# Optimization experiments

Measured on AMD Instinct MI355X. Metric: run time of the kernel, lower is better.

The kernel has to match this reference:

```python
import jax, jax.numpy as jnp
import numpy as np
from jax import lax

B = 8192
HS = 64        # hidden_size (output channels)
HS4 = HS + 4   # internal channel count (68)
K = 3          # conv kernel size


def setup_inputs() -> dict:
    key = jax.random.key(0)
    ks = jax.random.split(key, 16)
    def n(k, shape, s=1.0):
        return jax.random.normal(k, shape, dtype=jnp.float32) * s
    return {
        "x": n(ks[0], (B, HS, 6, 6)),
        "cell": n(ks[1], (B, 2)),
        "interspace_coord": n(ks[2], (B, 2, 6, 6)),
        "conv1_w": n(ks[3], (HS4, HS4, K, K), 0.05),
        "conv1_b": n(ks[4], (HS4,), 0.05),
        "conv3_w": n(ks[5], (HS4, HS4, K, K), 0.05),
        "conv3_b": n(ks[6], (HS4,), 0.05),
        "lin5_w": n(ks[7], (9 * HS, HS4 * 25), 0.02),
        "lin5_b": n(ks[8], (9 * HS,), 0.02),
        "lin4_w": n(ks[9], (9 * HS, HS4 * 16), 0.02),
        "lin4_b": n(ks[10], (9 * HS,), 0.02),
        "lin3_w": n(ks[11], (9 * HS, HS4 * 9), 0.02),
        "lin3_b": n(ks[12], (9 * HS,), 0.02),
        "final_w": n(ks[13], (HS, 9 * HS), 0.02),
        "final_b": n(ks[14], (HS,), 0.02),
    }


def _conv(z, w, b):
    # torch Conv2d with padding=k//2, stride 1 == SAME conv, NCHW/OIHW
    y = lax.conv_general_dilated(z, w, (1, 1), 'SAME',
                                 dimension_numbers=('NCHW', 'OIHW', 'NCHW'))
    return y + b[None, :, None, None]


def _corners(z, ws):
    # four corner windows, stacked on a new leading axis (corner-major)
    H, W = z.shape[-2:]
    return jnp.stack([z[..., :ws, :ws],
                      z[..., :ws, W - ws:],
                      z[..., H - ws:, :ws],
                      z[..., H - ws:, W - ws:]], axis=0)


def reference(x, cell, interspace_coord,
              conv1_w, conv1_b, conv3_w, conv3_b,
              lin5_w, lin5_b, lin4_w, lin4_b, lin3_w, lin3_b,
              final_w, final_b):
    Bn = x.shape[0]
    new_cell = jnp.broadcast_to(cell.reshape(Bn, -1)[:, :, None, None],
                                (Bn, 2, 6, 6))
    lins = {5: (lin5_w, lin5_b), 4: (lin4_w, lin4_b), 3: (lin3_w, lin3_b)}
    for ws in (5, 4, 3):
        z = jnp.concatenate([x, new_cell, interspace_coord], axis=1)  # [B,68,6,6]
        z = _corners(z, ws).reshape(-1, HS4, ws, ws)                  # [4B,68,ws,ws]
        z = jnp.sin(z) + jnp.cos(z)
        z = jax.nn.relu(_conv(z, conv1_w, conv1_b))
        z = jnp.sin(z) + jnp.cos(z)
        z = jax.nn.relu(_conv(z, conv3_w, conv3_b)).reshape(4, Bn, -1)
        Wl, bl = lins[ws]
        z = jax.nn.relu(z @ Wl.T + bl).reshape(4, Bn, HS, 3, 3)
        m = jnp.concatenate([z[0], z[1]], axis=-1)   # [B,64,3,6]
        n = jnp.concatenate([z[2], z[3]], axis=-1)
        x = jnp.concatenate([m, n], axis=-2)          # [B,64,6,6]
    ew = 3
    c = _corners(x, ew)                               # [4,B,64,3,3]
    c = c.reshape(4 * Bn, -1) @ final_w.T + final_b   # [4B,64]
    c = c.reshape(Bn, HS, 2, 2)                       # same flat-order reshape as torch
    xc = x[:, :, ew - 1:ew + 1, ew - 1:ew + 1]        # center 2x2
    return (xc * c).reshape(Bn, HS, -1)
```

## Files before the change

kernel.cpp:

```cpp
#include <hip/hip_runtime.h>
#include <hip/hip_bf16.h>
#include <cstdint>
#include <cstddef>

#define BN 8192
#define MTOT 32768

using bf16 = __hip_bfloat16;
typedef float f32x4 __attribute__((ext_vector_type(4)));
typedef short short8 __attribute__((ext_vector_type(8)));

__device__ __forceinline__ bf16 f2b(float v) { return __float2bfloat16(v); }
__device__ __forceinline__ float b2f(bf16 v) { return __bfloat162float(v); }
__device__ __forceinline__ float sincos_sum(float x) {
    return 1.41421356237f * __sinf(x + 0.78539816340f);
}

template<int WS> struct WsCfg;
template<> struct WsCfg<5> { static constexpr int KD = 1728, NP = 1792, KTRUE = 1700; };
template<> struct WsCfg<4> { static constexpr int KD = 1088, NP = 1152, KTRUE = 1088; };
template<> struct WsCfg<3> { static constexpr int KD = 640,  NP = 640,  KTRUE = 612;  };

__global__ __launch_bounds__(256)
void zprep_block(const float* __restrict__ xF, const float* __restrict__ cell,
                 const float* __restrict__ isc, bf16* __restrict__ Z,
                 int m0g, int CM)
{
    constexpr int KD = 1728, KTRUE = 1700;
    const int b = blockIdx.x, tid = threadIdx.x;
    __shared__ float s[68][37];

    for (int i = tid; i < 64 * 36; i += 256) {
        int ic = i / 36, off = i % 36;
        s[ic][off] = sincos_sum(xF[((size_t)b * 64 + ic) * 36 + off]);
    }
    if (tid < 2) {
        float t = sincos_sum(cell[b * 2 + tid]);
        #pragma unroll
        for (int off = 0; off < 36; off++) s[64 + tid][off] = t;
    }
    if (tid >= 64 && tid < 136) {
        int j = tid - 64;
        int ic = j / 36, off = j % 36;
        s[66 + ic][off] = sincos_sum(isc[((size_t)b * 2 + ic) * 36 + off]);
    }
    __syncthreads();

    for (int i = tid; i < 4 * KD; i += 256) {
        int q = i / KD, k = i % KD;
        int gm = q * BN + b;
        if (gm < m0g || gm >= m0g + CM) continue;
        float v = 0.f;
        if (k < KTRUE) {
            int pi = k / 68, ic = k % 68;
            int r = (q >> 1) + pi / 5;
            int c = (q & 1) + pi % 5;
            v = s[ic][r * 6 + c];
        }
        Z[(size_t)(gm - m0g) * KD + k] = f2b(v);
    }
}

template<int WSv>
__device__ __forceinline__ bf16 conv_elem(const float* __restrict__ src, int n, int k)
{
    constexpr int KTRUE = 68 * WSv * WSv;
    float v = 0.f;
    if (n < KTRUE && k < KTRUE) {
        int po = n / 68, oc = n % 68, ro = po / WSv, co = po % WSv;
        int pi = k / 68, ic = k % 68, ri = pi / WSv, ci = pi % WSv;
        int kr = ri - ro + 1, kc = ci - co + 1;
        if (kr >= 0 && kr < 3 && kc >= 0 && kc < 3)
            v = src[((oc * 68 + ic) * 3 + kr) * 3 + kc];
    }
    return f2b(v);
}
template<int WSv>
__device__ __forceinline__ bf16 lin_elem(const float* __restrict__ wl, int n, int k)
{
    constexpr int KTRUE = 68 * WSv * WSv;
    float v = 0.f;
    if (n < 576 && k < KTRUE) {
        int pi = k / 68, ic = k % 68;
        v = wl[(size_t)n * KTRUE + ic * (WSv * WSv) + pi];
    }
    return f2b(v);
}

__global__ void megabuild(const float* __restrict__ c1w, const float* __restrict__ c3w,
                          const float* __restrict__ l5w, const float* __restrict__ l4w,
                          const float* __restrict__ l3w, const float* __restrict__ fw,
                          const float* __restrict__ c1b, const float* __restrict__ c3b,
                          const float* __restrict__ bl5, const float* __restrict__ bl4,
                          const float* __restrict__ bl3, const float* __restrict__ bfin,
                          const float* __restrict__ cell, const float* __restrict__ isc,
                          bf16* __restrict__ w1d5, bf16* __restrict__ w3d5,
                          bf16* __restrict__ w1d4, bf16* __restrict__ w3d4,
                          bf16* __restrict__ w1d3, bf16* __restrict__ w3d3,
                          bf16* __restrict__ wl5p, bf16* __restrict__ wl4p,
                          bf16* __restrict__ wl3p, bf16* __restrict__ wfp,
                          float* __restrict__ bias,
                          bf16* __restrict__ Z4, bf16* __restrict__ Z3)
{
    constexpr unsigned S0 = 2u*1792*1728, S1 = 2u*1152*1088, S2 = 2u*640*640;
    constexpr unsigned S3 = 640u*1728, S4 = 640u*1088, S5 = 640u*640;
    constexpr unsigned S6 = 128u*576, S7 = 9216;
    constexpr unsigned S8 = 4u*8192*16*4, S9 = 4u*8192*9*4, S10 = 32768u*28;
    constexpr unsigned O1=S0, O2=O1+S1, O3=O2+S2, O4=O3+S3, O5=O4+S4, O6=O5+S5,
                       O7=O6+S6, O8=O7+S7, O9=O8+S8, O10=O9+S9, OT=O10+S10;
    unsigned e = blockIdx.x * 256u + threadIdx.x;
    if (e >= OT) return;
    if (e < O1) {
        constexpr unsigned per = 1792u*1728;
        unsigned i = (e < per) ? e : e - per;
        bf16* dst = (e < per) ? w1d5 : w3d5;
        const float* src = (e < per) ? c1w : c3w;
        dst[i] = conv_elem<5>(src, (int)(i / 1728u), (int)(i % 1728u));
    } else if (e < O2) {
        unsigned i0 = e - O1; constexpr unsigned per = 1152u*1088;
        unsigned i = (i0 < per) ? i0 : i0 - per;
        bf16* dst = (i0 < per) ? w1d4 : w3d4;
        const float* src = (i0 < per) ? c1w : c3w;
        dst[i] = conv_elem<4>(src, (int)(i / 1088u), (int)(i % 1088u));
    } else if (e < O3) {
        unsigned i0 = e - O2; constexpr unsigned per = 640u*640;
        unsigned i = (i0 < per) ? i0 : i0 - per;
        bf16* dst = (i0 < per) ? w1d3 : w3d3;
        const float* src = (i0 < per) ? c1w : c3w;
        dst[i] = conv_elem<3>(src, (int)(i / 640u), (int)(i % 640u));
    } else if (e < O4) {
        unsigned i = e - O3;
        wl5p[i] = lin_elem<5>(l5w, (int)(i / 1728u), (int)(i % 1728u));
    } else if (e < O5) {
        unsigned i = e - O4;
        wl4p[i] = lin_elem<4>(l4w, (int)(i / 1088u), (int)(i % 1088u));
    } else if (e < O6) {
        unsigned i = e - O5;
        wl3p[i] = lin_elem<3>(l3w, (int)(i / 640u), (int)(i % 640u));
    } else if (e < O7) {
        unsigned i = e - O6, n = i / 576u, k = i % 576u;
        wfp[i] = (n < 64u) ? f2b(fw[n * 576u + k]) : f2b(0.f);
    } else if (e < O8) {
        int i = (int)(e - O7);
        float v = 0.f;
        if (i < 1792)      { int n = i;        if (n < 1700) v = c1b[n % 68]; }
        else if (i < 3584) { int n = i - 1792; if (n < 1700) v = c3b[n % 68]; }
        else if (i < 4736) { int n = i - 3584; if (n < 1088) v = c1b[n % 68]; }
        else if (i < 5888) { int n = i - 4736; if (n < 1088) v = c3b[n % 68]; }
        else if (i < 6528) { int n = i - 5888; if (n < 612)  v = c1b[n % 68]; }
        else if (i < 7168) { int n = i - 6528; if (n < 612)  v = c3b[n % 68]; }
        else if (i < 7808) { int n = i - 7168; if (n < 576)  v = bl5[n]; }
        else if (i < 8448) { int n = i - 7808; if (n < 576)  v = bl4[n]; }
        else if (i < 9088) { int n = i - 8448; if (n < 576)  v = bl3[n]; }
        else               { int n = i - 9088; if (n < 64)   v = bfin[n]; }
        bias[i] = v;
    } else if (e < O9) {
        unsigned i = e - O8;
        int j = (int)(i & 3u); i >>= 2;
        int pi = (int)(i & 15u); i >>= 4;
        int b = (int)(i & 8191u); int q = (int)(i >> 13);
        float t;
        if (j < 2) t = cell[b * 2 + j];
        else {
            int r = (q >> 1) * 2 + pi / 4, c = (q & 1) * 2 + pi % 4;
            t = isc[((size_t)b * 2 + (j - 2)) * 36 + r * 6 + c];
        }
        Z4[((size_t)q * BN + b) * 1088 + pi * 68 + 64 + j] = f2b(sincos_sum(t));
    } else if (e < O10) {
        unsigned i = e - O9;
        int j = (int)(i & 3u); i >>= 2;
        int pi = (int)(i % 9u); i /= 9u;
        int b = (int)(i & 8191u); int q = (int)(i >> 13);
        float t;
        if (j < 2) t = cell[b * 2 + j];
        else {
            int r = (q >> 1) * 3 + pi / 3, c = (q & 1) * 3 + pi % 3;
            t = isc[((size_t)b * 2 + (j - 2)) * 36 + r * 6 + c];
        }
        Z3[((size_t)q * BN + b) * 640 + pi * 68 + 64 + j] = f2b(sincos_sum(t));
    } else {
        unsigned i = e - O10;
        int m = (int)(i / 28u), t = (int)(i % 28u);
        Z3[(size_t)m * 640 + 612 + t] = f2b(0.f);
    }
}

__device__ __forceinline__ void gload_lds16(const bf16* g, const bf16* lds_wave_base)
{
    unsigned off = (unsigned)(uintptr_t)lds_wave_base;
    off = __builtin_amdgcn_readfirstlane(off);
    __builtin_amdgcn_global_load_lds((const __attribute__((address_space(1))) unsigned int*)g,
                                     (__attribute__((address_space(3))) unsigned int*)off,
                                     16, 0, 0);
}

__device__ __forceinline__ int imin(int a, int b) { return a < b ? a : b; }
__device__ __forceinline__ int imax(int a, int b) { return a > b ? a : b; }

template<int EPI, int WS, int WN>
__global__ __launch_bounds__(256)
void gemm_bt(const bf16* __restrict__ A, const bf16* __restrict__ Bm, int KD,
             const float* __restrict__ bias, int ntiles,
             bf16* __restrict__ C, int ldc, int nlimit,
             int m0g, bf16* __restrict__ znext,
             const bf16* __restrict__ afin_xc, float* __restrict__ outp)
{
    __shared__ bf16 As[128 * 32];
    __shared__ bf16 Bs[128 * 32];
    const int tid = threadIdx.x;
    const int wave = tid >> 6, lane = tid & 63;
    const int l15 = lane & 15, lq = lane >> 4;
    const int wr = (wave >> 1) * 64, wc = (wave & 1) * 64;

    const int id = blockIdx.x;
    const int mt8 = (int)gridDim.x / (ntiles * 8);
    const int xcd = id & 7, local = id >> 3;
    const int m_idx = xcd * mt8 + local / ntiles;
    const int n_idx = local % ntiles;
    const int n0 = n_idx * 128, m0 = m_idx * 128;

    int nspans = 1, sbeg[4], send[4];
    sbeg[0] = 0; send[0] = KD;
    if (WS > 0) {
        int po_lo = imin(n0 / 68, WS * WS - 1);
        int po_hi = imin((n0 + 127) / 68, WS * WS - 1);
        int ro_lo = po_lo / WS, ro_hi = po_hi / WS;
        int r_lo = imax(ro_lo - 1, 0), r_hi = imin(ro_hi + 1, WS - 1);
        int ci_lo = 0, ci_hi = WS - 1;
        if (ro_lo == ro_hi) {
            ci_lo = imax(po_lo % WS - 1, 0);
            ci_hi = imin(po_hi % WS + 1, WS - 1);
        }
        if (ci_lo == 0 && ci_hi == WS - 1) {
            sbeg[0] = (r_lo * WS * 68) & ~31;
            send[0] = imin(KD, ((r_hi + 1) * WS * 68 + 31) & ~31);
        } else {
            nspans = 0;
            for (int ri = r_lo; ri <= r_hi; ri++) {
                sbeg[nspans] = ((ri * WS + ci_lo) * 68) & ~31;
                send[nspans] = imin(KD, (((ri * WS + ci_hi + 1) * 68) + 31) & ~31);
                nspans++;
            }
        }
    }

    float bj[4];
    #pragma unroll
    for (int j = 0; j < 4; j++) bj[j] = bias[n0 + wc + j * 16 + l15];

    const bf16* Ab = A + (size_t)m0 * KD;
    const bf16* Bb = Bm + (size_t)n0 * KD;
    const int srow = tid >> 2, scol = (tid & 3) * 8;
    const bf16* aG0 = Ab + (size_t)srow * KD + scol;
    const bf16* aG1 = Ab + (size_t)(srow + 64) * KD + scol;
    const bf16* bG0 = Bb + (size_t)srow * KD + scol;
    const bf16* bG1 = Bb + (size_t)(srow + 64) * KD + scol;
    const bf16* lA0 = &As[wave * 512];
    const bf16* lA1 = &As[2048 + wave * 512];
    const bf16* lB0 = &Bs[wave * 512];
    const bf16* lB1 = &Bs[2048 + wave * 512];

    f32x4 acc[4][4];
    #pragma unroll
    for (int i = 0; i < 4; i++)
        #pragma unroll
        for (int j = 0; j < 4; j++) { f32x4 z = {0.f, 0.f, 0.f, 0.f}; acc[i][j] = z; }

    for (int s = 0; s < nspans; s++) {
        for (int k0 = sbeg[s]; k0 < send[s]; k0 += 32) {
            gload_lds16(aG0 + k0, lA0);
            gload_lds16(aG1 + k0, lA1);
            gload_lds16(bG0 + k0, lB0);
            gload_lds16(bG1 + k0, lB1);
            __syncthreads();
            short8 af[4], bg[4];
            #pragma unroll
            for (int i = 0; i < 4; i++) af[i] = *(const short8*)&As[(wr + i * 16 + l15) * 32 + lq * 8];
            #pragma unroll
            for (int j = 0; j < 4; j++) bg[j] = *(const short8*)&Bs[(wc + j * 16 + l15) * 32 + lq * 8];
            #pragma unroll
            for (int i = 0; i < 4; i++)
                #pragma unroll
                for (int j = 0; j < 4; j++)
                    acc[i][j] = __builtin_amdgcn_mfma_f32_16x16x32_bf16(af[i], bg[j], acc[i][j], 0, 0, 0);
            __syncthreads();
        }
    }

    #pragma unroll
    for (int i = 0; i < 4; i++) {
        #pragma unroll
        for (int j = 0; j < 4; j++) {
            int n = n0 + wc + j * 16 + l15;
            #pragma unroll
            for (int r = 0; r < 4; r++) {
                int m = m0 + wr + i * 16 + lq * 4 + r;
                float v = acc[i][j][r];
                if (EPI == 0) {
                    if (n < nlimit) {
                        v += bj[j]; v = fmaxf(v, 0.f); v = sincos_sum(v);
                        C[(size_t)m * ldc + n] = f2b(v);
                    }
                } else if (EPI == 1) {
                    if (n < nlimit) {
                        v += bj[j]; v = fmaxf(v, 0.f);
                        C[(size_t)m * ldc + n] = f2b(v);
                    }
                } else if (EPI == 2) {
                    if (n < 576) {
                        v += bj[j]; v = fmaxf(v, 0.f);
                        bf16 t = f2b(sincos_sum(v));
                        int gm = m0g + m;
                        int q = gm >> 13, b = gm & (BN - 1);
                        int ch = n / 9, p = n % 9;
                        int R = p / 3 + (q >> 1) * 3, Cc = p % 3 + (q & 1) * 3;
                        constexpr int OFF = 6 - WN;
                        constexpr int KDN = (WN == 4) ? 1088 : 640;
                        #pragma unroll
                        for (int qr = 0; qr < 2; qr++) {
                            int rr = R - OFF * qr;
                            if (rr < 0 || rr >= WN) continue;
                            #pragma unroll
                            for (int qc = 0; qc < 2; qc++) {
                                int cc = Cc - OFF * qc;
                                if (cc < 0 || cc >= WN) continue;
                                int pi = rr * WN + cc;
                                znext[((size_t)((qr * 2 + qc) * BN + b)) * KDN + pi * 68 + ch] = t;
                            }
                        }
                    }
                } else {
                    if (n < 64) {
                        v += bj[j];
                        int gm = m0g + m;
                        int f = gm * 64 + n;
                        int b2 = f >> 8, rem = f & 255;
                        int ch2 = rem >> 2, ii = (rem >> 1) & 1, jj = rem & 1;
                        int qq = ii * 2 + jj;
                        const int offt[4] = {8, 6, 2, 0};
                        float xc = b2f(afin_xc[((size_t)qq * BN + b2) * 576 + ch2 * 9 + offt[qq]]);
                        outp[f] = v * xc;
                    }
                }
            }
        }
    }
}

extern "C" void kernel_launch(void* const* d_in, const int* in_sizes, int n_in,
                              void* d_out, int out_size, void* d_ws, size_t ws_size,
                              hipStream_t stream)
{
    const float* x    = (const float*)d_in[0];
    const float* cell = (const float*)d_in[1];
    const float* isc  = (const float*)d_in[2];
    const float* c1w  = (const float*)d_in[3];
    const float* c1b  = (const float*)d_in[4];
    const float* c3w  = (const float*)d_in[5];
    const float* c3b  = (const float*)d_in[6];
    const float* l5w  = (const float*)d_in[7];
    const float* l5b  = (const float*)d_in[8];
    const float* l4w  = (const float*)d_in[9];
    const float* l4b  = (const float*)d_in[10];
    const float* l3w  = (const float*)d_in[11];
    const float* l3b  = (const float*)d_in[12];
    const float* fw   = (const float*)d_in[13];
    const float* fb   = (const float*)d_in[14];

    char* base = (char*)d_ws;
    size_t cur = 0;
    auto take = [&](size_t bytes) -> char* {
        char* r = base + cur; cur += (bytes + 255) & ~(size_t)255; return r;
    };

    const size_t Z4B = (size_t)MTOT * 1088 * 2;
    const size_t Z3B = (size_t)MTOT * 640 * 2;
    const size_t AFB = (size_t)MTOT * 576 * 2;
    size_t wbytes = 2 * (1792ull * 1728 + 1152ull * 1088 + 640ull * 640) * 2
                  + (640ull * 1728 + 640ull * 1088 + 640ull * 640) * 2
                  + 128ull * 576 * 2 + 9216ull * 4 + 64 * 256;
    auto need = [&](int nc) -> size_t {
        return Z4B + Z3B + AFB + wbytes + 2 * ((size_t)(MTOT / nc) * 1728 * 2);
    };
    int nchunk = (ws_size >= need(1)) ? 1 : (ws_size >= need(2)) ? 2
               : (ws_size >= need(4)) ? 4 : (ws_size >= need(8)) ? 8 : 16;

    bf16* Z4   = (bf16*)take(Z4B);
    bf16* Z3   = (bf16*)take(Z3B);
    bf16* afinb = (bf16*)take(AFB);
    bf16* w1d5 = (bf16*)take(1792ull * 1728 * 2);
    bf16* w3d5 = (bf16*)take(1792ull * 1728 * 2);
    bf16* w1d4 = (bf16*)take(1152ull * 1088 * 2);
    bf16* w3d4 = (bf16*)take(1152ull * 1088 * 2);
    bf16* w1d3 = (bf16*)take(640ull * 640 * 2);
    bf16* w3d3 = (bf16*)take(640ull * 640 * 2);
    bf16* wl5p = (bf16*)take(640ull * 1728 * 2);
    bf16* wl4p = (bf16*)take(640ull * 1088 * 2);
    bf16* wl3p = (bf16*)take(640ull * 640 * 2);
    bf16* wfp  = (bf16*)take(128ull * 576 * 2);
    float* biasb = (float*)take(9216ull * 4);
    int CM = MTOT / nchunk;
    int mt = CM / 128;
    bf16* Za = (bf16*)take((size_t)CM * 1728 * 2);
    bf16* Zb = (bf16*)take((size_t)CM * 1728 * 2);

    {
        constexpr unsigned OT = 2u*1792*1728 + 2u*1152*1088 + 2u*640*640
                              + 640u*1728 + 640u*1088 + 640u*640 + 128u*576 + 9216
                              + 4u*8192*16*4 + 4u*8192*9*4 + 32768u*28;
        megabuild<<<(OT + 255) / 256, 256, 0, stream>>>(
            c1w, c3w, l5w, l4w, l3w, fw, c1b, c3b, l5b, l4b, l3b, fb, cell, isc,
            w1d5, w3d5, w1d4, w3d4, w1d3, w3d3, wl5p, wl4p, wl3p, wfp, biasb, Z4, Z3);
    }

    for (int c = 0; c < nchunk; c++) {
        int m0g = c * CM;
        zprep_block<<<BN, 256, 0, stream>>>(x, cell, isc, Za, m0g, CM);
        gemm_bt<0, 5, 0><<<14 * mt, 256, 0, stream>>>(Za, w1d5, 1728, biasb + 0, 14,
                                                      Zb, 1728, 1728, 0, nullptr, nullptr, nullptr);
        gemm_bt<1, 5, 0><<<14 * mt, 256, 0, stream>>>(Zb, w3d5, 1728, biasb + 1792, 14,
                                                      Za, 1728, 1728, 0, nullptr, nullptr, nullptr);
        gemm_bt<2, 0, 4><<<5 * mt, 256, 0, stream>>>(Za, wl5p, 1728, biasb + 7168, 5,
                                                     nullptr, 0, 0, m0g, Z4, nullptr, nullptr);
    }
    for (int c = 0; c < nchunk; c++) {
        int m0g = c * CM;
        gemm_bt<0, 4, 0><<<9 * mt, 256, 0, stream>>>(Z4 + (size_t)m0g * 1088, w1d4, 1088,
                                                     biasb + 3584, 9, Zb, 1088, 1088,
                                                     0, nullptr, nullptr, nullptr);
        gemm_bt<1, 4, 0><<<9 * mt, 256, 0, stream>>>(Zb, w3d4, 1088, biasb + 4736, 9,
                                                     Za, 1088, 1088, 0, nullptr, nullptr, nullptr);
        gemm_bt<2, 0, 3><<<5 * mt, 256, 0, stream>>>(Za, wl4p, 1088, biasb + 7808, 5,
                                                     nullptr, 0, 0, m0g, Z3, nullptr, nullptr);
    }
    for (int c = 0; c < nchunk; c++) {
        int m0g = c * CM;
        gemm_bt<0, 3, 0><<<5 * mt, 256, 0, stream>>>(Z3 + (size_t)m0g * 640, w1d3, 640,
                                                     biasb + 5888, 5, Zb, 640, 640,
                                                     0, nullptr, nullptr, nullptr);
        gemm_bt<1, 3, 0><<<5 * mt, 256, 0, stream>>>(Zb, w3d3, 640, biasb + 6528, 5,
                                                     Za, 640, 640, 0, nullptr, nullptr, nullptr);
        gemm_bt<1, 0, 0><<<5 * mt, 256, 0, stream>>>(Za, wl3p, 640, biasb + 8448, 5,
                                                     afinb + (size_t)m0g * 576, 576, 576,
                                                     0, nullptr, nullptr, nullptr);
    }
    for (int c = 0; c < nchunk; c++) {
        int m0g = c * CM;
        gemm_bt<3, 0, 0><<<mt, 256, 0, stream>>>(afinb + (size_t)m0g * 576, wfp, 576,
                                                 biasb + 9088, 1, nullptr, 0, 0, m0g,
                                                 nullptr, afinb, (float*)d_out);
    }
}
```

Baseline: 1.340 ms.

## Stage GEMM epilogue through shared memory for coalesced vectorized stores

```diff
diff --git a/kernel.cpp b/kernel.cpp
--- a/kernel.cpp
+++ b/kernel.cpp
@@ -9,6 +9,7 @@
 using bf16 = __hip_bfloat16;
 typedef float f32x4 __attribute__((ext_vector_type(4)));
 typedef short short8 __attribute__((ext_vector_type(8)));
+typedef short short4v __attribute__((ext_vector_type(4)));
 
 __device__ __forceinline__ bf16 f2b(float v) { return __float2bfloat16(v); }
 __device__ __forceinline__ float b2f(bf16 v) { return __bfloat162float(v); }
@@ -205,8 +206,7 @@
              int m0g, bf16* __restrict__ znext,
              const bf16* __restrict__ afin_xc, float* __restrict__ outp)
 {
-    __shared__ bf16 As[128 * 32];
-    __shared__ bf16 Bs[128 * 32];
+    __shared__ bf16 smem[8192];
     const int tid = threadIdx.x;
     const int wave = tid >> 6, lane = tid & 63;
     const int l15 = lane & 15, lq = lane >> 4;
@@ -255,10 +255,10 @@
     const bf16* aG1 = Ab + (size_t)(srow + 64) * KD + scol;
     const bf16* bG0 = Bb + (size_t)srow * KD + scol;
     const bf16* bG1 = Bb + (size_t)(srow + 64) * KD + scol;
-    const bf16* lA0 = &As[wave * 512];
-    const bf16* lA1 = &As[2048 + wave * 512];
-    const bf16* lB0 = &Bs[wave * 512];
-    const bf16* lB1 = &Bs[2048 + wave * 512];
+    const bf16* lA0 = &smem[wave * 512];
+    const bf16* lA1 = &smem[2048 + wave * 512];
+    const bf16* lB0 = &smem[4096 + wave * 512];
+    const bf16* lB1 = &smem[4096 + 2048 + wave * 512];
 
     f32x4 acc[4][4];
     #pragma unroll
@@ -275,9 +275,9 @@
             __syncthreads();
             short8 af[4], bg[4];
             #pragma unroll
-            for (int i = 0; i < 4; i++) af[i] = *(const short8*)&As[(wr + i * 16 + l15) * 32 + lq * 8];
-            #pragma unroll
-            for (int j = 0; j < 4; j++) bg[j] = *(const short8*)&Bs[(wc + j * 16 + l15) * 32 + lq * 8];
+            for (int i = 0; i < 4; i++) af[i] = *(const short8*)&smem[(wr + i * 16 + l15) * 32 + lq * 8];
+            #pragma unroll
+            for (int j = 0; j < 4; j++) bg[j] = *(const short8*)&smem[4096 + (wc + j * 16 + l15) * 32 + lq * 8];
             #pragma unroll
             for (int i = 0; i < 4; i++)
                 #pragma unroll
@@ -287,51 +287,17 @@
         }
     }
 
-    #pragma unroll
-    for (int i = 0; i < 4; i++) {
+    if (EPI == 3) {
         #pragma unroll
-        for (int j = 0; j < 4; j++) {
-            int n = n0 + wc + j * 16 + l15;
-            #pragma unroll
-            for (int r = 0; r < 4; r++) {
-                int m = m0 + wr + i * 16 + lq * 4 + r;
-                float v = acc[i][j][r];
-                if (EPI == 0) {
-                    if (n < nlimit) {
-                        v += bj[j]; v = fmaxf(v, 0.f); v = sincos_sum(v);
-                        C[(size_t)m * ldc + n] = f2b(v);
-                    }
-                } else if (EPI == 1) {
-                    if (n < nlimit) {
-                        v += bj[j]; v = fmaxf(v, 0.f);
-                        C[(size_t)m * ldc + n] = f2b(v);
-                    }
-                } else if (EPI == 2) {
-                    if (n < 576) {
-                        v += bj[j]; v = fmaxf(v, 0.f);
-                        bf16 t = f2b(sincos_sum(v));
-                        int gm = m0g + m;
-                        int q = gm >> 13, b = gm & (BN - 1);
-                        int ch = n / 9, p = n % 9;
-                        int R = p / 3 + (q >> 1) * 3, Cc = p % 3 + (q & 1) * 3;
-                        constexpr int OFF = 6 - WN;
-                        constexpr int KDN = (WN == 4) ? 1088 : 640;
-                        #pragma unroll
-                        for (int qr = 0; qr < 2; qr++) {
-                            int rr = R - OFF * qr;
-                            if (rr < 0 || rr >= WN) continue;
-                            #pragma unroll
-                            for (int qc = 0; qc < 2; qc++) {
-                                int cc = Cc - OFF * qc;
-                                if (cc < 0 || cc >= WN) continue;
-                                int pi = rr * WN + cc;
-                                znext[((size_t)((qr * 2 + qc) * BN + b)) * KDN + pi * 68 + ch] = t;
-                            }
-                        }
-                    }
-                } else {
+        for (int i = 0; i < 4; i++) {
+            #pragma unroll
+            for (int j = 0; j < 4; j++) {
+                int n = n0 + wc + j * 16 + l15;
+                #pragma unroll
+                for (int r = 0; r < 4; r++) {
+                    int m = m0 + wr + i * 16 + lq * 4 + r;
                     if (n < 64) {
-                        v += bj[j];
+                        float v = acc[i][j][r] + bj[j];
                         int gm = m0g + m;
                         int f = gm * 64 + n;
                         int b2 = f >> 8, rem = f & 255;
@@ -342,6 +308,65 @@
                         outp[f] = v * xc;
                     }
                 }
+            }
+        }
+        return;
+    }
+
+    const int myh = wave >> 1;
+    for (int h = 0; h < 2; h++) {
+        __syncthreads();
+        if (myh == h) {
+            #pragma unroll
+            for (int i = 0; i < 4; i++)
+                #pragma unroll
+                for (int j = 0; j < 4; j++)
+                    #pragma unroll
+                    for (int r = 0; r < 4; r++) {
+                        float v = acc[i][j][r] + bj[j];
+                        v = fmaxf(v, 0.f);
+                        if (EPI != 1) v = sincos_sum(v);
+                        smem[(i * 16 + lq * 4 + r) * 128 + wc + j * 16 + l15] = f2b(v);
+                    }
+        }
+        __syncthreads();
+        if (EPI == 0 || EPI == 1) {
+            int row = tid >> 2, col0 = (tid & 3) * 32;
+            int m = m0 + h * 64 + row;
+            #pragma unroll
+            for (int c = 0; c < 4; c++) {
+                int n = n0 + col0 + c * 8;
+                if (n < nlimit)
+                    *(short8*)&C[(size_t)m * ldc + n] = *(const short8*)&smem[row * 128 + col0 + c * 8];
+            }
+        } else {
+            constexpr int OFF = 6 - WN;
+            constexpr int KDN = (WN == 4) ? 1088 : 640;
+            int nhi = imin(n0 + 128, 576);
+            for (int u = tid; u < 64 * 9 * 4; u += 256) {
+                int widx = u & 3, p = (u >> 2) % 9, lm = (u >> 2) / 9;
+                int gm = m0g + m0 + h * 64 + lm;
+                int q5 = gm >> 13, b = gm & (BN - 1);
+                int R = p / 3 + (q5 >> 1) * 3, Cc = p % 3 + (q5 & 1) * 3;
+                int rr = R - OFF * (widx >> 1);
+                int cc = Cc - OFF * (widx & 1);
+                if (rr < 0 || rr >= WN || cc < 0 || cc >= WN) continue;
+                int pi = rr * WN + cc;
+                bf16* dst = znext + ((size_t)(widx * BN + b)) * KDN + pi * 68;
+                int c0 = (n0 == 0) ? 0 : (n0 - p + 8) / 9;
+                int c1 = (nhi - 1 - p) / 9;
+                const bf16* src = &smem[lm * 128 + p - n0];
+                int ch = c0;
+                for (; ch <= c1 && (ch & 3); ch++) dst[ch] = src[ch * 9];
+                for (; ch + 3 <= c1; ch += 4) {
+                    short4v v;
+                    v.x = *(const short*)&src[ch * 9];
+                    v.y = *(const short*)&src[ch * 9 + 9];
+                    v.z = *(const short*)&src[ch * 9 + 18];
+                    v.w = *(const short*)&src[ch * 9 + 27];
+                    *(short4v*)&dst[ch] = v;
+                }
+                for (; ch <= c1; ch++) dst[ch] = src[ch * 9];
             }
         }
     }
```

After: 1.449 ms. 1.08x slower.
